# Kernel tuning notes

Measured on AMD Instinct MI355X. Metric: run time of the kernel, lower is better.

Reference implementation:

```python
import jax, jax.numpy as jnp
import numpy as np

B, S, D, H, DEG = 4, 2048, 1024, 4096, 4  # batch, seq, n_embd, hidden, chebyshev degree
LN_EPS = 1e-5


def cheb_basis(x, degree):
    """Chebyshev polynomials T_0..T_degree of x (values assumed in [-1,1]).
    x: [..., d] -> [..., d, degree+1] via the recurrence T_k = 2x T_{k-1} - T_{k-2}."""
    T = [jnp.ones_like(x), x]
    for _ in range(2, degree + 1):
        T.append(2.0 * x * T[-1] - T[-2])
    return jnp.stack(T[: degree + 1], axis=-1)


def kan_layer(x, coef, degree):
    # x: [N, in_dim], coef: [in_dim, out_dim, degree+1] -> [N, out_dim]
    basis = cheb_basis(x, degree)  # [N, in_dim, degree+1]
    return jnp.einsum('nik,iok->no', basis, coef)


def setup_inputs() -> dict:
    key = jax.random.key(0)
    k1, k2, k3 = jax.random.split(key, 3)
    x = jax.random.normal(k1, (B, S, D), dtype=jnp.float32)
    # Chebyshev-KAN coefficient init ~ N(0, 1/(in_dim*(degree+1)))
    coef_fc = jax.random.normal(k2, (D, H, DEG + 1), dtype=jnp.float32) / np.sqrt(D * (DEG + 1))
    coef_proj = jax.random.normal(k3, (H, D, DEG + 1), dtype=jnp.float32) / np.sqrt(H * (DEG + 1))
    gamma = jnp.ones((H,), dtype=jnp.float32)
    beta = jnp.zeros((H,), dtype=jnp.float32)
    return {"x": x, "coef_fc": coef_fc, "coef_proj": coef_proj, "gamma": gamma, "beta": beta}


def reference(x, coef_fc, coef_proj, gamma, beta):
    b, s, d = x.shape
    xf = jnp.tanh(x.reshape(-1, d))                 # squash into Chebyshev domain [-1,1]
    h = kan_layer(xf, coef_fc, DEG)                 # [N, H]
    mu = jnp.mean(h, axis=-1, keepdims=True)
    var = jnp.mean(jnp.square(h - mu), axis=-1, keepdims=True)
    h = (h - mu) * jax.lax.rsqrt(var + LN_EPS) * gamma + beta
    h = jnp.tanh(h)
    out = kan_layer(h, coef_proj, DEG)              # [N, D]
    return out.reshape(b, s, d)                     # dropout is identity at eval
```

## Files before the change

### kernel.cpp

```cpp
#include <hip/hip_runtime.h>
#include <hip/hip_bf16.h>
#include <cstdint>
#include <cstddef>

typedef __bf16 bf16;
typedef __attribute__((ext_vector_type(4))) __bf16 bf16x4;
typedef __attribute__((ext_vector_type(8))) __bf16 bf16x8;
typedef __attribute__((ext_vector_type(4))) float f32x4;

#define NR 8192
#define DIM_D 1024
#define DIM_H 4096


__device__ __forceinline__ void gload_lds16(const void* g, void* l) {
  __builtin_amdgcn_global_load_lds(
      (const __attribute__((address_space(1))) void*)g,
      (__attribute__((address_space(3))) void*)l, 16, 0, 0);
}

#define BAR()  __builtin_amdgcn_s_barrier()
#define WLG0() asm volatile("s_waitcnt lgkmcnt(0)" ::: "memory")
#define WVM0() asm volatile("s_waitcnt vmcnt(0)" ::: "memory")
#define WVM4() asm volatile("s_waitcnt vmcnt(4)" ::: "memory")
#define WVM6() asm volatile("s_waitcnt vmcnt(6)" ::: "memory")
#define WVM8() asm volatile("s_waitcnt vmcnt(8)" ::: "memory")
#define PRIO1() __builtin_amdgcn_s_setprio(1)
#define PRIO0() __builtin_amdgcn_s_setprio(0)


template <int IN, int OUT>
__global__ __launch_bounds__(256) void k_prep_t(const float* __restrict__ coef,
                                                bf16* __restrict__ Bp,
                                                float* __restrict__ bpart) {
  constexpr int KT = (IN / 32) * 2;
  const int tid   = threadIdx.x;
  const int o     = blockIdx.x * 256 + tid;
  const int nb    = blockIdx.x;
  const int chunk = blockIdx.y;
  const int i0    = chunk * 32;

  float bacc = 0.f;
#pragma unroll
  for (int q = 0; q < 4; ++q) {
    bf16x8 w1, w2, w3, w4;
#pragma unroll
    for (int j = 0; j < 8; ++j) {
      const float* s = coef + ((size_t)(i0 + q * 8 + j) * OUT + o) * 5;
      bacc += s[0];
      w1[j] = (bf16)s[1]; w2[j] = (bf16)s[2]; w3[j] = (bf16)s[3]; w4[j] = (bf16)s[4];
    }
    bf16* base = Bp + ((size_t)nb * KT + chunk * 2) * 16384 + (size_t)tid * 8;
    *(bf16x8*)(base + (0 * 4 + q) * 2048)         = w1;
    *(bf16x8*)(base + (1 * 4 + q) * 2048)         = w2;
    *(bf16x8*)(base + 16384 + (0 * 4 + q) * 2048) = w3;
    *(bf16x8*)(base + 16384 + (1 * 4 + q) * 2048) = w4;
  }
  bpart[(size_t)chunk * OUT + o] = bacc;
}

__global__ __launch_bounds__(256) void k_bias_red(const float* __restrict__ bpart,
                                                  float* __restrict__ bias,
                                                  const int OUT, const int NP) {
  const int o = blockIdx.x * 256 + threadIdx.x;
  float s = 0.f;
  for (int p = 0; p < NP; ++p) s += bpart[(size_t)p * OUT + o];
  bias[o] = s;
}

__global__ __launch_bounds__(256) void k_tanh_cheb(const float* __restrict__ x,
                                                   bf16* __restrict__ Ax) {
  const size_t base = ((size_t)blockIdx.x * 256 + threadIdx.x) * 8;
  const size_t row  = base >> 10;
  const int    i    = (int)(base & 1023);
  const float4 v0 = *(const float4*)(x + base);
  const float4 v1 = *(const float4*)(x + base + 4);
  float f[8] = {tanhf(v0.x), tanhf(v0.y), tanhf(v0.z), tanhf(v0.w),
                tanhf(v1.x), tanhf(v1.y), tanhf(v1.z), tanhf(v1.w)};
  bf16x8 w1, w2, w3, w4;
#pragma unroll
  for (int j = 0; j < 8; ++j) {
    const float a = f[j], a2 = a * a;
    w1[j] = (bf16)a;
    w2[j] = (bf16)(2.f * a2 - 1.f);
    w3[j] = (bf16)(a * (4.f * a2 - 3.f));
    w4[j] = (bf16)(8.f * a2 * (a2 - 1.f) + 1.f);
  }
  bf16* o = Ax + row * 4096 + (i >> 5) * 128 + ((i >> 3) & 3) * 8;
  *(bf16x8*)(o)      = w1;
  *(bf16x8*)(o + 32) = w2;
  *(bf16x8*)(o + 64) = w3;
  *(bf16x8*)(o + 96) = w4;
}

__global__ __launch_bounds__(256) void k_lntanh_cheb(const bf16* __restrict__ h,
                                                     const float* __restrict__ gamma,
                                                     const float* __restrict__ beta,
                                                     bf16* __restrict__ Ax) {
  const int n = blockIdx.x;
  const int t = threadIdx.x;
  const bf16* row = h + (size_t)n * DIM_H;

  float v[16];
  float s1 = 0.f, s2 = 0.f;
  {
    const bf16x8 a = *(const bf16x8*)(row + t * 16);
    const bf16x8 b = *(const bf16x8*)(row + t * 16 + 8);
#pragma unroll
    for (int j = 0; j < 8; ++j) { v[j] = (float)a[j]; v[8 + j] = (float)b[j]; }
#pragma unroll
    for (int j = 0; j < 16; ++j) { s1 += v[j]; s2 += v[j] * v[j]; }
  }
#pragma unroll
  for (int off = 32; off >= 1; off >>= 1) {
    s1 += __shfl_xor(s1, off);
    s2 += __shfl_xor(s2, off);
  }
  __shared__ float red[8];
  if ((t & 63) == 0) { red[(t >> 6) * 2] = s1; red[(t >> 6) * 2 + 1] = s2; }
  __syncthreads();
  const float S1 = red[0] + red[2] + red[4] + red[6];
  const float S2 = red[1] + red[3] + red[5] + red[7];
  const float mu   = S1 * (1.f / DIM_H);
  const float var  = S2 * (1.f / DIM_H) - mu * mu;
  const float rstd = rsqrtf(var + 1e-5f);

  float f[16];
#pragma unroll
  for (int j = 0; j < 16; ++j) {
    const float g = gamma[t * 16 + j];
    const float b = beta[t * 16 + j];
    f[j] = tanhf((v[j] - mu) * rstd * g + b);
  }
  bf16* o = Ax + (size_t)n * 16384 + (t >> 1) * 128 + ((t & 1) * 2) * 8;
#pragma unroll
  for (int k = 1; k <= 4; ++k) {
    bf16x8 w0, w1;
#pragma unroll
    for (int j = 0; j < 8; ++j) {
      const float a = f[j], a2 = a * a;
      const float b = f[8 + j], b2 = b * b;
      float ra, rb;
      if (k == 1)      { ra = a;                           rb = b; }
      else if (k == 2) { ra = 2.f * a2 - 1.f;              rb = 2.f * b2 - 1.f; }
      else if (k == 3) { ra = a * (4.f * a2 - 3.f);        rb = b * (4.f * b2 - 3.f); }
      else             { ra = 8.f * a2 * (a2 - 1.f) + 1.f; rb = 8.f * b2 * (b2 - 1.f) + 1.f; }
      w0[j] = (bf16)ra; w1[j] = (bf16)rb;
    }
    *(bf16x8*)(o + (k - 1) * 32)     = w0;
    *(bf16x8*)(o + (k - 1) * 32 + 8) = w1;
  }
}

__global__ __launch_bounds__(256) void k_ln_tanh(const float* __restrict__ h,
                                                 const float* __restrict__ gamma,
                                                 const float* __restrict__ beta,
                                                 bf16* __restrict__ th) {
  const int n = blockIdx.x;
  const int t = threadIdx.x;
  const float* row = h + (size_t)n * DIM_H;

  float4 v[4];
  float s1 = 0.f, s2 = 0.f;
#pragma unroll
  for (int j = 0; j < 4; ++j) {
    v[j] = *(const float4*)(row + t * 16 + j * 4);
    s1 += v[j].x + v[j].y + v[j].z + v[j].w;
    s2 += v[j].x * v[j].x + v[j].y * v[j].y + v[j].z * v[j].z + v[j].w * v[j].w;
  }
#pragma unroll
  for (int off = 32; off >= 1; off >>= 1) {
    s1 += __shfl_xor(s1, off);
    s2 += __shfl_xor(s2, off);
  }
  __shared__ float red[8];
  if ((t & 63) == 0) { red[(t >> 6) * 2] = s1; red[(t >> 6) * 2 + 1] = s2; }
  __syncthreads();
  const float S1 = red[0] + red[2] + red[4] + red[6];
  const float S2 = red[1] + red[3] + red[5] + red[7];
  const float mu   = S1 * (1.f / DIM_H);
  const float var  = S2 * (1.f / DIM_H) - mu * mu;
  const float rstd = rsqrtf(var + 1e-5f);

  float tmp[16];
#pragma unroll
  for (int j = 0; j < 4; ++j) {
    const float4 g = *(const float4*)(gamma + t * 16 + j * 4);
    const float4 b = *(const float4*)(beta  + t * 16 + j * 4);
    tmp[j * 4 + 0] = tanhf((v[j].x - mu) * rstd * g.x + b.x);
    tmp[j * 4 + 1] = tanhf((v[j].y - mu) * rstd * g.y + b.y);
    tmp[j * 4 + 2] = tanhf((v[j].z - mu) * rstd * g.z + b.z);
    tmp[j * 4 + 3] = tanhf((v[j].w - mu) * rstd * g.w + b.w);
  }
  bf16x8 w0, w1;
#pragma unroll
  for (int j = 0; j < 8; ++j) { w0[j] = (bf16)tmp[j]; w1[j] = (bf16)tmp[8 + j]; }
  bf16* o = th + (size_t)n * DIM_H + t * 16;
  *(bf16x8*)o       = w0;
  *(bf16x8*)(o + 8) = w1;
}

template <int IND, int NZ, typename CT>
__global__ __launch_bounds__(512, 2) void k_gemm8x(const bf16* __restrict__ Ax,
                                                   const bf16* __restrict__ Bp,
                                                   CT* __restrict__ C,
                                                   const float* __restrict__ bias,
                                                   const int NN) {
  constexpr int KP  = IND * 4;
  constexpr int NCH = IND / 32 / NZ;
  constexpr int KTt = (IND / 32) * 2;

  __shared__ bf16 Ash[2][16384];
  __shared__ bf16 Bsh[2][16384];

  const int tid  = threadIdx.x;
  const int lane = tid & 63;
  const int wid  = tid >> 6;
  const int wm   = wid >> 2;
  const int wn   = wid & 3;
  const int fr   = lane & 15;
  const int kq   = lane >> 4;
  const int m0   = blockIdx.y * 256;
  const int n0   = blockIdx.x * 256;
  const int zc0  = blockIdx.z * NCH;

  f32x4 acc[8][4];
#pragma unroll
  for (int m = 0; m < 8; ++m)
#pragma unroll
    for (int n = 0; n < 4; ++n) acc[m][n] = (f32x4){0.f, 0.f, 0.f, 0.f};

  const size_t bt0 = (size_t)blockIdx.x * KTt + (size_t)zc0 * 2;
  const bf16* Az = Ax + (size_t)zc0 * 128;

  const int sub = tid >> 8;
  const int rA  = tid & 255;

  auto stB = [&](int d, int kh, int ktl) {
    const bf16* s = Bp + (bt0 + (size_t)ktl) * 16384 + kh * 8192 + tid * 8;
    bf16* l = &Bsh[d][kh * 8192 + tid * 8];
    gload_lds16(s, l);
    gload_lds16(s + 4096, l + 4096);
  };
  auto stA = [&](int d, int kh, int ktl) {
    const bf16* s = Az + (size_t)(m0 + rA) * KP + (size_t)ktl * 64 + kh * 32 + sub * 8;
    bf16* l = &Ash[d][(kh * 4 + sub) * 2048 + rA * 8];
    gload_lds16(s, l);
    gload_lds16(s + 16, l + 4096);
  };

  bf16x8 afr[4], bfr[4];
  auto rdB = [&](int d, int kh) {
#pragma unroll
    for (int n = 0; n < 4; ++n)
      bfr[n] = *(const bf16x8*)&Bsh[d][(kh * 4 + kq) * 2048 + (wn * 64 + n * 16 + fr) * 8];
  };
  auto rdA = [&](int d, int kh, int mh) {
#pragma unroll
    for (int m = 0; m < 4; ++m)
      afr[m] = *(const bf16x8*)&Ash[d][(kh * 4 + kq) * 2048 + (wm * 128 + mh * 64 + m * 16 + fr) * 8];
  };
  auto mma = [&](int mh) {
#pragma unroll
    for (int m = 0; m < 4; ++m)
#pragma unroll
      for (int n = 0; n < 4; ++n)
        acc[mh * 4 + m][n] =
            __builtin_amdgcn_mfma_f32_16x16x32_bf16(afr[m], bfr[n], acc[mh * 4 + m][n], 0, 0, 0);
  };

  stA(0, 0, 0); stA(0, 1, 0); stB(0, 0, 0); stB(0, 1, 0);
  stA(1, 0, 1); stA(1, 1, 1); stB(1, 0, 1); stB(1, 1, 1);
  WVM8();
  BAR();

#pragma unroll 1
  for (int g = 0; g < NCH; ++g) {
    const bool st = (g + 1 < NCH);
    rdB(0, 0); rdA(0, 0, 0);
    if (g > 0) stA(1, 1, 2 * g + 1);
    BAR(); WLG0();
    PRIO1(); mma(0); PRIO0();
    BAR();
    rdA(0, 0, 1);
    if (st) stB(0, 0, 2 * g + 2);
    BAR(); WLG0();
    PRIO1(); mma(1); PRIO0();
    BAR();
    rdB(0, 1); rdA(0, 1, 0);
    if (st) stA(0, 0, 2 * g + 2);
    BAR(); WLG0();
    PRIO1(); mma(0); PRIO0();
    BAR();
    rdA(0, 1, 1);
    if (st) { stB(0, 1, 2 * g + 2); WVM6(); } else { WVM0(); }
    BAR(); WLG0();
    PRIO1(); mma(1); PRIO0();
    BAR();
    rdB(1, 0); rdA(1, 0, 0);
    if (st) stA(0, 1, 2 * g + 2);
    BAR(); WLG0();
    PRIO1(); mma(0); PRIO0();
    BAR();
    rdA(1, 0, 1);
    if (st) stB(1, 0, 2 * g + 3);
    BAR(); WLG0();
    PRIO1(); mma(1); PRIO0();
    BAR();
    rdB(1, 1); rdA(1, 1, 0);
    if (st) stA(1, 0, 2 * g + 3);
    BAR(); WLG0();
    PRIO1(); mma(0); PRIO0();
    BAR();
    rdA(1, 1, 1);
    if (st) { stB(1, 1, 2 * g + 3); WVM6(); }
    BAR(); WLG0();
    PRIO1(); mma(1); PRIO0();
    BAR();
  }

  float bv[4] = {0.f, 0.f, 0.f, 0.f};
  const int c0 = n0 + wn * 64 + fr;
  if (bias) {
#pragma unroll
    for (int n = 0; n < 4; ++n) bv[n] = bias[c0 + n * 16];
  }
  CT* Cz = C + (size_t)blockIdx.z * NR * NN;
  const int r0 = m0 + wm * 128 + kq * 4;
#pragma unroll
  for (int mi = 0; mi < 8; ++mi)
#pragma unroll
    for (int j = 0; j < 4; ++j) {
      CT* p = Cz + (size_t)(r0 + mi * 16 + j) * NN + c0;
#pragma unroll
      for (int n = 0; n < 4; ++n)
        p[n * 16] = (CT)(acc[mi][n][j] + bv[n]);
    }
}

template <int IND, int NZ>
__global__ __launch_bounds__(512, 2) void k_gemm8(const bf16* __restrict__ X,
                                                  const bf16* __restrict__ Bp,
                                                  float* __restrict__ C,
                                                  const float* __restrict__ bias,
                                                  const int NN) {
  constexpr int NCH = IND / 32 / NZ;
  constexpr int KTt = (IND / 32) * 2;

  __shared__ bf16 Ash[2][16384];
  __shared__ bf16 Bsh[2][16384];

  const int tid  = threadIdx.x;
  const int lane = tid & 63;
  const int wid  = tid >> 6;
  const int wm   = wid >> 2;
  const int wn   = wid & 3;
  const int fr   = lane & 15;
  const int kq   = lane >> 4;
  const int m0   = blockIdx.y * 256;
  const int n0   = blockIdx.x * 256;
  const int zc0  = blockIdx.z * NCH;

  const int ar = tid >> 1;
  const int aq = (tid & 1) * 2;

  f32x4 acc[8][4];
#pragma unroll
  for (int m = 0; m < 8; ++m)
#pragma unroll
    for (int n = 0; n < 4; ++n) acc[m][n] = (f32x4){0.f, 0.f, 0.f, 0.f};

  const bf16* xp = X + (size_t)(m0 + ar) * IND + (size_t)zc0 * 32 + aq * 8;
  const size_t bt0 = (size_t)blockIdx.x * KTt + (size_t)zc0 * 2;

  bf16x8 xn0, xn1;
  float  xf[16];
  bf16x8 afr[4], bfr[4];

  auto stB = [&](int d, int kh, int ktl) {
    const bf16* s = Bp + (bt0 + (size_t)ktl) * 16384 + kh * 8192 + tid * 8;
    bf16* l = &Bsh[d][kh * 8192 + tid * 8];
    gload_lds16(s, l);
    gload_lds16(s + 4096, l + 4096);
  };
  auto ldx = [&](int c) {
    const bf16* s = xp + (size_t)c * 32;
    xn0 = *(const bf16x8*)s;
    xn1 = *(const bf16x8*)(s + 8);
  };
  auto cvtxf = [&]() {
#pragma unroll
    for (int j = 0; j < 8; ++j) { xf[j] = (float)xn0[j]; xf[8 + j] = (float)xn1[j]; }
  };
  auto wA = [&](int d, int dh, bf16x8 w0, bf16x8 w1) {
    *(bf16x8*)&Ash[d][(dh * 4 + aq) * 2048 + ar * 8]       = w0;
    *(bf16x8*)&Ash[d][(dh * 4 + aq + 1) * 2048 + ar * 8]   = w1;
  };
  auto chebw = [&](int deg, bf16x8& w0, bf16x8& w1) {
#pragma unroll
    for (int j = 0; j < 8; ++j) {
      const float a = xf[j], b = xf[8 + j];
      const float a2 = a * a, b2 = b * b;
      float ra, rb;
      if (deg == 2)      { ra = 2.f * a2 - 1.f;            rb = 2.f * b2 - 1.f; }
      else if (deg == 3) { ra = a * (4.f * a2 - 3.f);      rb = b * (4.f * b2 - 3.f); }
      else               { ra = 8.f * a2 * (a2 - 1.f) + 1.f; rb = 8.f * b2 * (b2 - 1.f) + 1.f; }
      w0[j] = (bf16)ra; w1[j] = (bf16)rb;
    }
  };
  auto rdB = [&](int d, int kh) {
#pragma unroll
    for (int n = 0; n < 4; ++n)
      bfr[n] = *(const bf16x8*)&Bsh[d][(kh * 4 + kq) * 2048 + (wn * 64 + n * 16 + fr) * 8];
  };
  auto rdA = [&](int d, int kh, int mh) {
#pragma unroll
    for (int m = 0; m < 4; ++m)
      afr[m] = *(const bf16x8*)&Ash[d][(kh * 4 + kq) * 2048 + (wm * 128 + mh * 64 + m * 16 + fr) * 8];
  };
  auto mma = [&](int mh) {
#pragma unroll
    for (int m = 0; m < 4; ++m)
#pragma unroll
      for (int n = 0; n < 4; ++n)
        acc[mh * 4 + m][n] =
            __builtin_amdgcn_mfma_f32_16x16x32_bf16(afr[m], bfr[n], acc[mh * 4 + m][n], 0, 0, 0);
  };

  ldx(0);
  stB(0, 0, 0); stB(0, 1, 0);
  stB(1, 0, 1); stB(1, 1, 1);
  cvtxf();
  wA(0, 0, xn0, xn1);
  { bf16x8 w0, w1; chebw(2, w0, w1); wA(0, 1, w0, w1); }
  { bf16x8 w0, w1; chebw(3, w0, w1); wA(1, 0, w0, w1); }
  { bf16x8 w0, w1; chebw(4, w0, w1); wA(1, 1, w0, w1); }
  WVM0(); WLG0();
  BAR();

#pragma unroll 1
  for (int g = 0; g < NCH; ++g) {
    const bool st = (g + 1 < NCH);
    rdB(0, 0); rdA(0, 0, 0);
    if (g > 0) { bf16x8 w0, w1; chebw(4, w0, w1); wA(1, 1, w0, w1); }
    if (st) ldx(g + 1);
    BAR(); WLG0();
    PRIO1(); mma(0); PRIO0();
    BAR();
    rdA(0, 0, 1);
    if (st) stB(0, 0, 2 * (g + 1));
    BAR(); WLG0();
    PRIO1(); mma(1); PRIO0();
    BAR();
    rdB(0, 1); rdA(0, 1, 0);
    BAR(); WLG0();
    PRIO1(); mma(0); PRIO0();
    BAR();
    rdA(0, 1, 1);
    if (st) { stB(0, 1, 2 * (g + 1)); WVM6(); } else { WVM0(); }
    BAR(); WLG0();
    PRIO1(); mma(1); PRIO0();
    BAR();
    rdB(1, 0); rdA(1, 0, 0);
    if (st) { cvtxf(); wA(0, 0, xn0, xn1); }
    BAR(); WLG0();
    PRIO1(); mma(0); PRIO0();
    BAR();
    rdA(1, 0, 1);
    if (st) { bf16x8 w0, w1; chebw(2, w0, w1); wA(0, 1, w0, w1); }
    BAR(); WLG0();
    PRIO1(); mma(1); PRIO0();
    BAR();
    rdB(1, 1); rdA(1, 1, 0);
    if (st) { bf16x8 w0, w1; chebw(3, w0, w1); wA(1, 0, w0, w1); stB(1, 0, 2 * (g + 1) + 1); }
    BAR(); WLG0();
    PRIO1(); mma(0); PRIO0();
    BAR();
    rdA(1, 1, 1);
    if (st) { stB(1, 1, 2 * (g + 1) + 1); WVM4(); }
    BAR(); WLG0();
    PRIO1(); mma(1); PRIO0();
    BAR();
  }

  float bv[4] = {0.f, 0.f, 0.f, 0.f};
  const int c0 = n0 + wn * 64 + fr;
  if (bias) {
#pragma unroll
    for (int n = 0; n < 4; ++n) bv[n] = bias[c0 + n * 16];
  }
  float* Cz = C + (size_t)blockIdx.z * NR * NN;
  const int r0 = m0 + wm * 128 + kq * 4;
#pragma unroll
  for (int mi = 0; mi < 8; ++mi)
#pragma unroll
    for (int j = 0; j < 4; ++j) {
      float* p = Cz + (size_t)(r0 + mi * 16 + j) * NN + c0;
#pragma unroll
      for (int n = 0; n < 4; ++n)
        p[n * 16] = acc[mi][n][j] + bv[n];
    }
}

__global__ __launch_bounds__(256) void k_reduce2(const float* __restrict__ p0,
                                                 const float* __restrict__ p1,
                                                 const float* __restrict__ bias,
                                                 float* __restrict__ out) {
  const size_t base = (size_t)blockIdx.x * 1024 + threadIdx.x * 4;
  const float4 a = *(const float4*)(p0 + base);
  const float4 b = *(const float4*)(p1 + base);
  const float4 c = *(const float4*)(bias + threadIdx.x * 4);
  float4 r;
  r.x = a.x + b.x + c.x;
  r.y = a.y + b.y + c.y;
  r.z = a.z + b.z + c.z;
  r.w = a.w + b.w + c.w;
  *(float4*)(out + base) = r;
}


extern "C" void kernel_launch(void* const* d_in, const int* in_sizes, int n_in,
                              void* d_out, int out_size, void* d_ws, size_t ws_size,
                              hipStream_t stream) {
  const float* x         = (const float*)d_in[0];
  const float* coef_fc   = (const float*)d_in[1];
  const float* coef_proj = (const float*)d_in[2];
  const float* gamma     = (const float*)d_in[3];
  const float* beta      = (const float*)d_in[4];
  float* out = (float*)d_out;

  const size_t SZ_B   = (size_t)DIM_H * 4 * DIM_D * 2;
  const size_t SZ_A1  = (size_t)NR * DIM_D * 4 * 2;
  const size_t SZ_HB  = (size_t)NR * DIM_H * 2;
  const size_t SZ_HF  = (size_t)NR * DIM_H * 4;
  const size_t SZ_A2  = (size_t)NR * DIM_H * 4 * 2;
  const size_t SZ_BP1 = (size_t)32 * DIM_H * 4;
  const size_t SZ_BP2 = (size_t)128 * DIM_D * 4;

  char* w = (char*)d_ws;
  bf16*  B2p   = (bf16*)w;   w += SZ_B;
  float* bias1 = (float*)w;  w += DIM_H * 4;
  float* bias2 = (float*)w;  w += DIM_D * 4;
  char*  hbase = w;

  const size_t NEED_A = (size_t)(hbase - (char*)d_ws) + SZ_HB + SZ_A2;
  const bool EXP = (ws_size >= NEED_A);

  char* region = hbase + (EXP ? SZ_HB : SZ_HF);
  bf16*  A1x    = (bf16*)region;
  bf16*  B1p    = (bf16*)(region + SZ_A1);
  float* bpart1 = (float*)(region + SZ_A1 + SZ_B);
  float* bpart2 = (float*)(region + SZ_A1 + SZ_B + SZ_BP1);

  k_prep_t<DIM_D, DIM_H><<<dim3(DIM_H / 256, DIM_D / 32), 256, 0, stream>>>(coef_fc, B1p, bpart1);
  k_prep_t<DIM_H, DIM_D><<<dim3(DIM_D / 256, DIM_H / 32), 256, 0, stream>>>(coef_proj, B2p, bpart2);
  k_bias_red<<<DIM_H / 256, 256, 0, stream>>>(bpart1, bias1, DIM_H, DIM_D / 32);
  k_bias_red<<<DIM_D / 256, 256, 0, stream>>>(bpart2, bias2, DIM_D, DIM_H / 32);

  k_tanh_cheb<<<NR * DIM_D / 2048, 256, 0, stream>>>(x, A1x);

  if (EXP) {
    bf16*  h    = (bf16*)hbase;
    bf16*  A2x  = (bf16*)region;
    float* part = (float*)hbase;
    k_gemm8x<DIM_D, 1, bf16><<<dim3(DIM_H / 256, NR / 256, 1), 512, 0, stream>>>(
        A1x, B1p, h, bias1, DIM_H);
    k_lntanh_cheb<<<NR, 256, 0, stream>>>(h, gamma, beta, A2x);
    k_gemm8x<DIM_H, 2, float><<<dim3(DIM_D / 256, NR / 256, 2), 512, 0, stream>>>(
        A2x, B2p, part, nullptr, DIM_D);
    k_reduce2<<<NR, 256, 0, stream>>>(part, part + (size_t)NR * DIM_D, bias2, out);
  } else {
    float* h    = (float*)hbase;
    bf16*  th   = A1x;
    float* part = (float*)hbase;
    k_gemm8x<DIM_D, 1, float><<<dim3(DIM_H / 256, NR / 256, 1), 512, 0, stream>>>(
        A1x, B1p, h, bias1, DIM_H);
    k_ln_tanh<<<NR, 256, 0, stream>>>(h, gamma, beta, th);
    k_gemm8<DIM_H, 2><<<dim3(DIM_D / 256, NR / 256, 2), 512, 0, stream>>>(
        th, B2p, part, nullptr, DIM_D);
    k_reduce2<<<NR, 256, 0, stream>>>(part, part + (size_t)NR * DIM_D, bias2, out);
  }
}
```

Before: 768.4 us.

## Pre-tile first-layer Chebyshev operand and remap GEMM blocks across XCDs

The first-stage tanh+Chebyshev kernel now writes its A operand in the same 16384-element tile layout as B, so the first GEMM loads A with contiguous tile copies instead of strided row reads. Both GEMMs remap block indices so that consecutive launched blocks spread across the 8 chiplets with contiguous work per chiplet, which should improve L2 reuse. The bf16 intermediate path (EXP) is removed, leaving a single path that keeps the fp32 hidden state and the fused LN+tanh+Chebyshev inside the second GEMM. This costs more intermediate memory traffic in exchange for better load patterns.

```diff
diff --git a/kernel.cpp b/kernel.cpp
--- a/kernel.cpp
+++ b/kernel.cpp
@@ -68,48 +68,56 @@
   bias[o] = s;
 }
 
-__global__ __launch_bounds__(256) void k_tanh_cheb(const float* __restrict__ x,
-                                                   bf16* __restrict__ Ax) {
-  const size_t base = ((size_t)blockIdx.x * 256 + threadIdx.x) * 8;
-  const size_t row  = base >> 10;
-  const int    i    = (int)(base & 1023);
-  const float4 v0 = *(const float4*)(x + base);
-  const float4 v1 = *(const float4*)(x + base + 4);
-  float f[8] = {tanhf(v0.x), tanhf(v0.y), tanhf(v0.z), tanhf(v0.w),
-                tanhf(v1.x), tanhf(v1.y), tanhf(v1.z), tanhf(v1.w)};
-  bf16x8 w1, w2, w3, w4;
-#pragma unroll
-  for (int j = 0; j < 8; ++j) {
-    const float a = f[j], a2 = a * a;
-    w1[j] = (bf16)a;
-    w2[j] = (bf16)(2.f * a2 - 1.f);
-    w3[j] = (bf16)(a * (4.f * a2 - 3.f));
-    w4[j] = (bf16)(8.f * a2 * (a2 - 1.f) + 1.f);
-  }
-  bf16* o = Ax + row * 4096 + (i >> 5) * 128 + ((i >> 3) & 3) * 8;
-  *(bf16x8*)(o)      = w1;
-  *(bf16x8*)(o + 32) = w2;
-  *(bf16x8*)(o + 64) = w3;
-  *(bf16x8*)(o + 96) = w4;
-}
-
-__global__ __launch_bounds__(256) void k_lntanh_cheb(const bf16* __restrict__ h,
-                                                     const float* __restrict__ gamma,
-                                                     const float* __restrict__ beta,
-                                                     bf16* __restrict__ Ax) {
+__global__ __launch_bounds__(256) void k_tanh_cheb_t(const float* __restrict__ x,
+                                                     bf16* __restrict__ Ap) {
+  const int mb    = blockIdx.x;
+  const int chunk = blockIdx.y;
+  const int r     = threadIdx.x;
+
+  const float* src = x + (size_t)(mb * 256 + r) * DIM_D + chunk * 32;
+  float a[32];
+#pragma unroll
+  for (int u = 0; u < 8; ++u) {
+    const float4 v = *(const float4*)(src + u * 4);
+    a[u * 4 + 0] = tanhf(v.x);
+    a[u * 4 + 1] = tanhf(v.y);
+    a[u * 4 + 2] = tanhf(v.z);
+    a[u * 4 + 3] = tanhf(v.w);
+  }
+  bf16* base = Ap + ((size_t)mb * 64 + chunk * 2) * 16384 + (size_t)r * 8;
+#pragma unroll
+  for (int q = 0; q < 4; ++q) {
+    bf16x8 w1, w2, w3, w4;
+#pragma unroll
+    for (int j = 0; j < 8; ++j) {
+      const float t = a[q * 8 + j], t2 = t * t;
+      w1[j] = (bf16)t;
+      w2[j] = (bf16)(2.f * t2 - 1.f);
+      w3[j] = (bf16)(t * (4.f * t2 - 3.f));
+      w4[j] = (bf16)(8.f * t2 * (t2 - 1.f) + 1.f);
+    }
+    *(bf16x8*)(base + (0 * 4 + q) * 2048)         = w1;
+    *(bf16x8*)(base + (1 * 4 + q) * 2048)         = w2;
+    *(bf16x8*)(base + 16384 + (0 * 4 + q) * 2048) = w3;
+    *(bf16x8*)(base + 16384 + (1 * 4 + q) * 2048) = w4;
+  }
+}
+
+__global__ __launch_bounds__(256) void k_ln_tanh(const float* __restrict__ h,
+                                                 const float* __restrict__ gamma,
+                                                 const float* __restrict__ beta,
+                                                 bf16* __restrict__ th) {
   const int n = blockIdx.x;
   const int t = threadIdx.x;
-  const bf16* row = h + (size_t)n * DIM_H;
-
-  float v[16];
+  const float* row = h + (size_t)n * DIM_H;
+
+  float4 v[4];
   float s1 = 0.f, s2 = 0.f;
-  {
-    const bf16x8 a = *(const bf16x8*)(row + t * 16);
-    const bf16x8 b = *(const bf16x8*)(row + t * 16 + 8);
-#pragma unroll
-    for (int j = 0; j < 8; ++j) { v[j] = (float)a[j]; v[8 + j] = (float)b[j]; }
-#pragma unroll
-    for (int j = 0; j < 16; ++j) { s1 += v[j]; s2 += v[j] * v[j]; }
+#pragma unroll
+  for (int j = 0; j < 4; ++j) {
+    v[j] = *(const float4*)(row + t * 16 + j * 4);
+    s1 += v[j].x + v[j].y + v[j].z + v[j].w;
+    s2 += v[j].x * v[j].x + v[j].y * v[j].y + v[j].z * v[j].z + v[j].w * v[j].w;
   }
 #pragma unroll
   for (int off = 32; off >= 1; off >>= 1) {
@@ -125,63 +133,6 @@
   const float var  = S2 * (1.f / DIM_H) - mu * mu;
   const float rstd = rsqrtf(var + 1e-5f);
 
-  float f[16];
-#pragma unroll
-  for (int j = 0; j < 16; ++j) {
-    const float g = gamma[t * 16 + j];
-    const float b = beta[t * 16 + j];
-    f[j] = tanhf((v[j] - mu) * rstd * g + b);
-  }
-  bf16* o = Ax + (size_t)n * 16384 + (t >> 1) * 128 + ((t & 1) * 2) * 8;
-#pragma unroll
-  for (int k = 1; k <= 4; ++k) {
-    bf16x8 w0, w1;
-#pragma unroll
-    for (int j = 0; j < 8; ++j) {
-      const float a = f[j], a2 = a * a;
-      const float b = f[8 + j], b2 = b * b;
-      float ra, rb;
-      if (k == 1)      { ra = a;                           rb = b; }
-      else if (k == 2) { ra = 2.f * a2 - 1.f;              rb = 2.f * b2 - 1.f; }
-      else if (k == 3) { ra = a * (4.f * a2 - 3.f);        rb = b * (4.f * b2 - 3.f); }
-      else             { ra = 8.f * a2 * (a2 - 1.f) + 1.f; rb = 8.f * b2 * (b2 - 1.f) + 1.f; }
-      w0[j] = (bf16)ra; w1[j] = (bf16)rb;
-    }
-    *(bf16x8*)(o + (k - 1) * 32)     = w0;
-    *(bf16x8*)(o + (k - 1) * 32 + 8) = w1;
-  }
-}
-
-__global__ __launch_bounds__(256) void k_ln_tanh(const float* __restrict__ h,
-                                                 const float* __restrict__ gamma,
-                                                 const float* __restrict__ beta,
-                                                 bf16* __restrict__ th) {
-  const int n = blockIdx.x;
-  const int t = threadIdx.x;
-  const float* row = h + (size_t)n * DIM_H;
-
-  float4 v[4];
-  float s1 = 0.f, s2 = 0.f;
-#pragma unroll
-  for (int j = 0; j < 4; ++j) {
-    v[j] = *(const float4*)(row + t * 16 + j * 4);
-    s1 += v[j].x + v[j].y + v[j].z + v[j].w;
-    s2 += v[j].x * v[j].x + v[j].y * v[j].y + v[j].z * v[j].z + v[j].w * v[j].w;
-  }
-#pragma unroll
-  for (int off = 32; off >= 1; off >>= 1) {
-    s1 += __shfl_xor(s1, off);
-    s2 += __shfl_xor(s2, off);
-  }
-  __shared__ float red[8];
-  if ((t & 63) == 0) { red[(t >> 6) * 2] = s1; red[(t >> 6) * 2 + 1] = s2; }
-  __syncthreads();
-  const float S1 = red[0] + red[2] + red[4] + red[6];
-  const float S2 = red[1] + red[3] + red[5] + red[7];
-  const float mu   = S1 * (1.f / DIM_H);
-  const float var  = S2 * (1.f / DIM_H) - mu * mu;
-  const float rstd = rsqrtf(var + 1e-5f);
-
   float tmp[16];
 #pragma unroll
   for (int j = 0; j < 4; ++j) {
@@ -200,15 +151,16 @@
   *(bf16x8*)(o + 8) = w1;
 }
 
-template <int IND, int NZ, typename CT>
-__global__ __launch_bounds__(512, 2) void k_gemm8x(const bf16* __restrict__ Ax,
+template <int IND, int NZ, int GX, typename CT>
+__global__ __launch_bounds__(512, 2) void k_gemm8x(const bf16* __restrict__ Ap,
                                                    const bf16* __restrict__ Bp,
                                                    CT* __restrict__ C,
                                                    const float* __restrict__ bias,
                                                    const int NN) {
-  constexpr int KP  = IND * 4;
   constexpr int NCH = IND / 32 / NZ;
   constexpr int KTt = (IND / 32) * 2;
+  constexpr int TOT = GX * 32 * NZ;
+  constexpr int CPX = TOT / 8;
 
   __shared__ bf16 Ash[2][16384];
   __shared__ bf16 Bsh[2][16384];
@@ -220,9 +172,16 @@
   const int wn   = wid & 3;
   const int fr   = lane & 15;
   const int kq   = lane >> 4;
-  const int m0   = blockIdx.y * 256;
-  const int n0   = blockIdx.x * 256;
-  const int zc0  = blockIdx.z * NCH;
+
+  int lin = blockIdx.x + GX * (blockIdx.y + 32 * blockIdx.z);
+  lin = (lin & 7) * CPX + (lin >> 3);
+  const int bx = lin % GX;
+  const int by = (lin / GX) % 32;
+  const int bz = lin / (GX * 32);
+
+  const int m0  = by * 256;
+  const int n0  = bx * 256;
+  const int zc0 = bz * NCH;
 
   f32x4 acc[8][4];
 #pragma unroll
@@ -230,11 +189,8 @@
 #pragma unroll
     for (int n = 0; n < 4; ++n) acc[m][n] = (f32x4){0.f, 0.f, 0.f, 0.f};
 
-  const size_t bt0 = (size_t)blockIdx.x * KTt + (size_t)zc0 * 2;
-  const bf16* Az = Ax + (size_t)zc0 * 128;
-
-  const int sub = tid >> 8;
-  const int rA  = tid & 255;
+  const size_t bt0 = (size_t)bx * KTt + (size_t)zc0 * 2;
+  const size_t at0 = (size_t)by * KTt + (size_t)zc0 * 2;
 
   auto stB = [&](int d, int kh, int ktl) {
     const bf16* s = Bp + (bt0 + (size_t)ktl) * 16384 + kh * 8192 + tid * 8;
@@ -243,10 +199,10 @@
     gload_lds16(s + 4096, l + 4096);
   };
   auto stA = [&](int d, int kh, int ktl) {
-    const bf16* s = Az + (size_t)(m0 + rA) * KP + (size_t)ktl * 64 + kh * 32 + sub * 8;
-    bf16* l = &Ash[d][(kh * 4 + sub) * 2048 + rA * 8];
+    const bf16* s = Ap + (at0 + (size_t)ktl) * 16384 + kh * 8192 + tid * 8;
+    bf16* l = &Ash[d][kh * 8192 + tid * 8];
     gload_lds16(s, l);
-    gload_lds16(s + 16, l + 4096);
+    gload_lds16(s + 4096, l + 4096);
   };
 
   bf16x8 afr[4], bfr[4];
@@ -325,7 +281,7 @@
 #pragma unroll
     for (int n = 0; n < 4; ++n) bv[n] = bias[c0 + n * 16];
   }
-  CT* Cz = C + (size_t)blockIdx.z * NR * NN;
+  CT* Cz = C + (size_t)bz * NR * NN;
   const int r0 = m0 + wm * 128 + kq * 4;
 #pragma unroll
   for (int mi = 0; mi < 8; ++mi)
@@ -338,7 +294,7 @@
     }
 }
 
-template <int IND, int NZ>
+template <int IND, int NZ, int GX>
 __global__ __launch_bounds__(512, 2) void k_gemm8(const bf16* __restrict__ X,
                                                   const bf16* __restrict__ Bp,
                                                   float* __restrict__ C,
@@ -346,6 +302,8 @@
                                                   const int NN) {
   constexpr int NCH = IND / 32 / NZ;
   constexpr int KTt = (IND / 32) * 2;
+  constexpr int TOT = GX * 32 * NZ;
+  constexpr int CPX = TOT / 8;
 
   __shared__ bf16 Ash[2][16384];
   __shared__ bf16 Bsh[2][16384];
@@ -357,12 +315,19 @@
   const int wn   = wid & 3;
   const int fr   = lane & 15;
   const int kq   = lane >> 4;
-  const int m0   = blockIdx.y * 256;
-  const int n0   = blockIdx.x * 256;
-  const int zc0  = blockIdx.z * NCH;
-
-  const int ar = tid >> 1;
-  const int aq = (tid & 1) * 2;
+
+  int lin = blockIdx.x + GX * (blockIdx.y + 32 * blockIdx.z);
+  lin = (lin & 7) * CPX + (lin >> 3);
+  const int bx = lin % GX;
+  const int by = (lin / GX) % 32;
+  const int bz = lin / (GX * 32);
+
+  const int m0  = by * 256;
+  const int n0  = bx * 256;
+  const int zc0 = bz * NCH;
+
+  const int rA = tid & 255;
+  const int qp = (tid >> 8) * 2;
 
   f32x4 acc[8][4];
 #pragma unroll
@@ -370,8 +335,8 @@
 #pragma unroll
     for (int n = 0; n < 4; ++n) acc[m][n] = (f32x4){0.f, 0.f, 0.f, 0.f};
 
-  const bf16* xp = X + (size_t)(m0 + ar) * IND + (size_t)zc0 * 32 + aq * 8;
-  const size_t bt0 = (size_t)blockIdx.x * KTt + (size_t)zc0 * 2;
+  const bf16* xp = X + (size_t)(m0 + rA) * IND + (size_t)zc0 * 32 + qp * 8;
+  const size_t bt0 = (size_t)bx * KTt + (size_t)zc0 * 2;
 
   bf16x8 xn0, xn1;
   float  xf[16];
@@ -393,8 +358,8 @@
     for (int j = 0; j < 8; ++j) { xf[j] = (float)xn0[j]; xf[8 + j] = (float)xn1[j]; }
   };
   auto wA = [&](int d, int dh, bf16x8 w0, bf16x8 w1) {
-    *(bf16x8*)&Ash[d][(dh * 4 + aq) * 2048 + ar * 8]       = w0;
-    *(bf16x8*)&Ash[d][(dh * 4 + aq + 1) * 2048 + ar * 8]   = w1;
+    *(bf16x8*)&Ash[d][(dh * 4 + qp) * 2048 + rA * 8]     = w0;
+    *(bf16x8*)&Ash[d][(dh * 4 + qp + 1) * 2048 + rA * 8] = w1;
   };
   auto chebw = [&](int deg, bf16x8& w0, bf16x8& w1) {
 #pragma unroll
@@ -489,7 +454,7 @@
 #pragma unroll
     for (int n = 0; n < 4; ++n) bv[n] = bias[c0 + n * 16];
   }
-  float* Cz = C + (size_t)blockIdx.z * NR * NN;
+  float* Cz = C + (size_t)bz * NR * NN;
   const int r0 = m0 + wm * 128 + kq * 4;
 #pragma unroll
   for (int mi = 0; mi < 8; ++mi)
@@ -529,55 +494,36 @@
   const float* beta      = (const float*)d_in[4];
   float* out = (float*)d_out;
 
-  const size_t SZ_B   = (size_t)DIM_H * 4 * DIM_D * 2;
-  const size_t SZ_A1  = (size_t)NR * DIM_D * 4 * 2;
-  const size_t SZ_HB  = (size_t)NR * DIM_H * 2;
-  const size_t SZ_HF  = (size_t)NR * DIM_H * 4;
-  const size_t SZ_A2  = (size_t)NR * DIM_H * 4 * 2;
-  const size_t SZ_BP1 = (size_t)32 * DIM_H * 4;
-  const size_t SZ_BP2 = (size_t)128 * DIM_D * 4;
+  const size_t SZ_B  = (size_t)DIM_H * 4 * DIM_D * 2;
+  const size_t SZ_A1 = (size_t)NR * DIM_D * 4 * 2;
+  const size_t SZ_HF = (size_t)NR * DIM_H * 4;
 
   char* w = (char*)d_ws;
   bf16*  B2p   = (bf16*)w;   w += SZ_B;
   float* bias1 = (float*)w;  w += DIM_H * 4;
   float* bias2 = (float*)w;  w += DIM_D * 4;
-  char*  hbase = w;
-
-  const size_t NEED_A = (size_t)(hbase - (char*)d_ws) + SZ_HB + SZ_A2;
-  const bool EXP = (ws_size >= NEED_A);
-
-  char* region = hbase + (EXP ? SZ_HB : SZ_HF);
-  bf16*  A1x    = (bf16*)region;
-  bf16*  B1p    = (bf16*)(region + SZ_A1);
-  float* bpart1 = (float*)(region + SZ_A1 + SZ_B);
-  float* bpart2 = (float*)(region + SZ_A1 + SZ_B + SZ_BP1);
+  float* h     = (float*)w;  w += SZ_HF;
+  bf16*  A1p   = (bf16*)w;   w += SZ_A1;
+  bf16*  B1p   = (bf16*)w;   w += SZ_B;
+  float* bpart1 = (float*)w; w += (size_t)32 * DIM_H * 4;
+  float* bpart2 = (float*)w; w += (size_t)128 * DIM_D * 4;
+
+  float* part = h;
+  bf16*  th   = A1p;
 
   k_prep_t<DIM_D, DIM_H><<<dim3(DIM_H / 256, DIM_D / 32), 256, 0, stream>>>(coef_fc, B1p, bpart1);
   k_prep_t<DIM_H, DIM_D><<<dim3(DIM_D / 256, DIM_H / 32), 256, 0, stream>>>(coef_proj, B2p, bpart2);
   k_bias_red<<<DIM_H / 256, 256, 0, stream>>>(bpart1, bias1, DIM_H, DIM_D / 32);
   k_bias_red<<<DIM_D / 256, 256, 0, stream>>>(bpart2, bias2, DIM_D, DIM_H / 32);
 
-  k_tanh_cheb<<<NR * DIM_D / 2048, 256, 0, stream>>>(x, A1x);
-
-  if (EXP) {
-    bf16*  h    = (bf16*)hbase;
-    bf16*  A2x  = (bf16*)region;
-    float* part = (float*)hbase;
-    k_gemm8x<DIM_D, 1, bf16><<<dim3(DIM_H / 256, NR / 256, 1), 512, 0, stream>>>(
-        A1x, B1p, h, bias1, DIM_H);
-    k_lntanh_cheb<<<NR, 256, 0, stream>>>(h, gamma, beta, A2x);
-    k_gemm8x<DIM_H, 2, float><<<dim3(DIM_D / 256, NR / 256, 2), 512, 0, stream>>>(
-        A2x, B2p, part, nullptr, DIM_D);
-    k_reduce2<<<NR, 256, 0, stream>>>(part, part + (size_t)NR * DIM_D, bias2, out);
-  } else {
-    float* h    = (float*)hbase;
-    bf16*  th   = A1x;
-    float* part = (float*)hbase;
-    k_gemm8x<DIM_D, 1, float><<<dim3(DIM_H / 256, NR / 256, 1), 512, 0, stream>>>(
-        A1x, B1p, h, bias1, DIM_H);
-    k_ln_tanh<<<NR, 256, 0, stream>>>(h, gamma, beta, th);
-    k_gemm8<DIM_H, 2><<<dim3(DIM_D / 256, NR / 256, 2), 512, 0, stream>>>(
-        th, B2p, part, nullptr, DIM_D);
-    k_reduce2<<<NR, 256, 0, stream>>>(part, part + (size_t)NR * DIM_D, bias2, out);
-  }
-}
+  k_tanh_cheb_t<<<dim3(NR / 256, DIM_D / 32), 256, 0, stream>>>(x, A1p);
+
+  k_gemm8x<DIM_D, 1, 16, float><<<dim3(DIM_H / 256, NR / 256, 1), 512, 0, stream>>>(
+      A1p, B1p, h, bias1, DIM_H);
+
+  k_ln_tanh<<<NR, 256, 0, stream>>>(h, gamma, beta, th);
+
+  k_gemm8<DIM_H, 2, 4><<<dim3(DIM_D / 256, NR / 256, 2), 512, 0, stream>>>(
+      th, B2p, part, nullptr, DIM_D);
+  k_reduce2<<<NR, 256, 0, stream>>>(part, part + (size_t)NR * DIM_D, bias2, out);
+}
```

New measurement: 687.5 us. -10.5%, faster.
